# Kernel optimization log

Measured on AMD Instinct MI355X. Metric: run time of the kernel, lower is better.

The kernel has to match this reference:

```python
import jax, jax.numpy as jnp
import numpy as np
import math

B, T, C = 2, 2048, 2048
H = 16
HS = C // H            # 128
NLQ = 512              # q latent dim
NLKV = 512             # kv latent dim
RHD = 64               # rope head dim


def _rope(x, cos, sin):
    # x: [B,T,H,D], cos/sin: [T,D/2]; rotate consecutive pairs (re,im)
    b, t, h, d = x.shape
    xr = x.reshape(b, t, h, d // 2, 2)
    x_re, x_im = xr[..., 0], xr[..., 1]
    c = cos[None, :, None, :]
    s = sin[None, :, None, :]
    o_re = x_re * c - x_im * s
    o_im = x_re * s + x_im * c
    return jnp.stack([o_re, o_im], axis=-1).reshape(b, t, h, d)


def setup_inputs() -> dict:
    key = jax.random.key(0)
    ks = jax.random.split(key, 9)
    std = 0.02
    x = jax.random.normal(ks[0], (B, T, C), dtype=jnp.float32)
    # RoPE tables (rotary base 10000) for rope_head_dim
    inv_freq = 1.0 / (10000.0 ** (np.arange(0, RHD, 2, dtype=np.float32) / RHD))
    tpos = np.arange(T, dtype=np.float32)
    ang = np.outer(tpos, inv_freq)  # [T, RHD/2]
    freqs_cos = jnp.asarray(np.cos(ang), dtype=jnp.float32)
    freqs_sin = jnp.asarray(np.sin(ang), dtype=jnp.float32)
    W_dq = std * jax.random.normal(ks[1], (NLQ, C), dtype=jnp.float32)
    W_uq = std * jax.random.normal(ks[2], (C, NLQ), dtype=jnp.float32)
    W_dkv = std * jax.random.normal(ks[3], (NLKV, C), dtype=jnp.float32)
    W_uk = std * jax.random.normal(ks[4], (C, NLKV), dtype=jnp.float32)
    W_uv = std * jax.random.normal(ks[5], (C, NLKV), dtype=jnp.float32)
    W_qr = std * jax.random.normal(ks[6], (H * RHD, NLQ), dtype=jnp.float32)
    W_kr = std * jax.random.normal(ks[7], (RHD, C), dtype=jnp.float32)
    W_o = std * jax.random.normal(ks[8], (C, C), dtype=jnp.float32)
    return {"x": x, "freqs_cos": freqs_cos, "freqs_sin": freqs_sin,
            "W_dq": W_dq, "W_uq": W_uq, "W_dkv": W_dkv, "W_uk": W_uk,
            "W_uv": W_uv, "W_qr": W_qr, "W_kr": W_kr, "W_o": W_o}


def reference(x, freqs_cos, freqs_sin, W_dq, W_uq, W_dkv, W_uk, W_uv, W_qr, W_kr, W_o):
    b, t, c = x.shape
    # latent projections
    c_q = x @ W_dq.T                                   # [B,T,NLQ]
    q_c = (c_q @ W_uq.T).reshape(b, t, H, HS)          # content query
    c_kv = x @ W_dkv.T                                 # [B,T,NLKV]
    k_c = (c_kv @ W_uk.T).reshape(b, t, H, HS)         # content key
    v = (c_kv @ W_uv.T).reshape(b, t, H, HS)           # value
    # decoupled RoPE parts
    q_r = _rope((c_q @ W_qr.T).reshape(b, t, H, RHD), freqs_cos, freqs_sin)
    k_r = _rope((x @ W_kr.T).reshape(b, t, 1, RHD), freqs_cos, freqs_sin)
    k_r = jnp.broadcast_to(k_r, (b, t, H, RHD))        # shared across heads
    q = jnp.concatenate([q_c, q_r], axis=-1)           # [B,T,H,HS+RHD]
    k = jnp.concatenate([k_c, k_r], axis=-1)
    scale = 1.0 / math.sqrt(HS + RHD)
    scores = jnp.einsum('bqhd,bkhd->bhqk', q, k) * scale
    mask = jnp.tril(jnp.ones((t, t), dtype=bool))
    scores = jnp.where(mask[None, None], scores, jnp.finfo(scores.dtype).min)
    attn = jax.nn.softmax(scores, axis=-1)
    out = jnp.einsum('bhqk,bkhd->bqhd', attn, v).reshape(b, t, c)
    return out @ W_o.T
```

## Files before the change

### kernel.cpp

```cpp
#include <hip/hip_runtime.h>
#include <math.h>

#define B_ 2
#define T_ 2048
#define C_ 2048
#define H_ 16
#define HS_ 128
#define RHD_ 64

typedef _Float16 f16;
typedef f16 half8 __attribute__((ext_vector_type(8)));
typedef f16 half4v __attribute__((ext_vector_type(4)));
typedef f16 half2v __attribute__((ext_vector_type(2)));
typedef float f32x4 __attribute__((ext_vector_type(4)));

using gvoid_t = const __attribute__((address_space(1))) void;
using lvoid_t = __attribute__((address_space(3))) void;

#define GLOAD_LDS(gp, lp) \
  __builtin_amdgcn_global_load_lds((gvoid_t*)(gp), (lvoid_t*)(lp), 16, 0, 0)

struct ConvBatch {
  const float* src[9];
  f16* dst[9];
  int n[9];
};

__global__ __launch_bounds__(256) void conv_f32_f16_batch(ConvBatch args) {
  const int t = blockIdx.y;
  const float* __restrict__ s = args.src[t];
  f16* __restrict__ d = args.dst[t];
  const int n4 = args.n[t] >> 2;
  for (int i = blockIdx.x * blockDim.x + threadIdx.x; i < n4;
       i += gridDim.x * blockDim.x) {
    float4 v = ((const float4*)s)[i];
    half4v h = {(f16)v.x, (f16)v.y, (f16)v.z, (f16)v.w};
    ((half4v*)d)[i] = h;
  }
}

template <int BM, int BN, bool OUTF32>
__global__ __launch_bounds__(256) void gemm_nt(const f16* __restrict__ A,
                                               const f16* __restrict__ Bw,
                                               void* __restrict__ Cv, int M,
                                               int N, int K, float alpha) {
  constexpr int MF = BM / 32;
  constexpr int NF = BN / 32;
  __shared__ f16 As[2][BM * 32];
  __shared__ f16 Bs[2][BN * 32];
  const int tid = threadIdx.x;
  const int wid = tid >> 6;
  const int lane = tid & 63;
  const int l15 = lane & 15, lg = lane >> 4;
  const int wr = wid >> 1, wc = wid & 1;
  const long bm = (long)blockIdx.y * BM;
  const long bn = (long)blockIdx.x * BN;

  const f16* Ag = A + (bm + (tid >> 2)) * (long)K + (tid & 3) * 8;
  const f16* Bg = Bw + (bn + (tid >> 2)) * (long)K + (tid & 3) * 8;

  auto stg = [&](int p, int k0) {
#pragma unroll
    for (int c = 0; c < BM / 64; ++c)
      GLOAD_LDS(Ag + (long)c * 64 * K + k0, &As[p][wid * 512 + c * 2048]);
#pragma unroll
    for (int c = 0; c < BN / 64; ++c)
      GLOAD_LDS(Bg + (long)c * 64 * K + k0, &Bs[p][wid * 512 + c * 2048]);
  };

  f32x4 acc[MF][NF];
  const f32x4 zero = {0.f, 0.f, 0.f, 0.f};
#pragma unroll
  for (int m = 0; m < MF; ++m)
#pragma unroll
    for (int n = 0; n < NF; ++n) acc[m][n] = zero;

  stg(0, 0);
  __syncthreads();

  int cur = 0;
  for (int k0 = 0; k0 < K; k0 += 32) {
    if (k0 + 32 < K) stg(cur ^ 1, k0 + 32);
    half8 af[MF], bf[NF];
#pragma unroll
    for (int m = 0; m < MF; ++m)
      af[m] =
          *(const half8*)&As[cur][(wr * (BM / 2) + m * 16 + l15) * 32 + lg * 8];
#pragma unroll
    for (int n = 0; n < NF; ++n)
      bf[n] =
          *(const half8*)&Bs[cur][(wc * (BN / 2) + n * 16 + l15) * 32 + lg * 8];
    __builtin_amdgcn_s_setprio(1);
#pragma unroll
    for (int m = 0; m < MF; ++m)
#pragma unroll
      for (int n = 0; n < NF; ++n)
        acc[m][n] =
            __builtin_amdgcn_mfma_f32_16x16x32_f16(af[m], bf[n], acc[m][n], 0, 0, 0);
    __builtin_amdgcn_s_setprio(0);
    __syncthreads();
    cur ^= 1;
  }

#pragma unroll
  for (int m = 0; m < MF; ++m) {
#pragma unroll
    for (int n = 0; n < NF; ++n) {
#pragma unroll
      for (int r = 0; r < 4; ++r) {
        long row = bm + wr * (BM / 2) + m * 16 + lg * 4 + r;
        long col = bn + wc * (BN / 2) + n * 16 + l15;
        float v = acc[m][n][r] * alpha;
        if constexpr (OUTF32)
          ((float*)Cv)[row * N + col] = v;
        else
          ((f16*)Cv)[row * N + col] = (f16)v;
      }
    }
  }
}

__global__ __launch_bounds__(256) void rope_q_kernel(
    const f16* __restrict__ src, const float* __restrict__ cs,
    const float* __restrict__ sn, f16* __restrict__ dst, float scale) {
  int idx = blockIdx.x * blockDim.x + threadIdx.x;
  if (idx >= B_ * T_ * H_ * 32) return;
  int j = idx & 31;
  int t = (idx >> 9) & (T_ - 1);
  half2v v = *(const half2v*)(src + (size_t)idx * 2);
  float c = cs[t * 32 + j], s = sn[t * 32 + j];
  float re = (float)v[0], im = (float)v[1];
  half2v o2 = {(f16)((re * c - im * s) * scale),
               (f16)((re * s + im * c) * scale)};
  *(half2v*)(dst + (size_t)idx * 2) = o2;
}

__global__ __launch_bounds__(256) void rope_k_kernel(
    const f16* __restrict__ src, const float* __restrict__ cs,
    const float* __restrict__ sn, f16* __restrict__ dst) {
  int idx = blockIdx.x * blockDim.x + threadIdx.x;
  if (idx >= B_ * T_ * 32) return;
  int j = idx & 31;
  int t = (idx >> 5) & (T_ - 1);
  half2v v = *(const half2v*)(src + (size_t)idx * 2);
  float c = cs[t * 32 + j], s = sn[t * 32 + j];
  float re = (float)v[0], im = (float)v[1];
  half2v o2 = {(f16)(re * c - im * s), (f16)(re * s + im * c)};
  *(half2v*)(dst + (size_t)idx * 2) = o2;
}

__global__ __launch_bounds__(256) void transpose_v_kernel(
    const f16* __restrict__ v, f16* __restrict__ vt) {
  __shared__ f16 tile[64][64];
  const int t0 = blockIdx.x * 64, d0 = blockIdx.y * 64;
  const int bh = blockIdx.z, b = bh >> 4, h = bh & 15;
  const int rr = threadIdx.x >> 3, cc = (threadIdx.x & 7) * 8;
#pragma unroll
  for (int p = 0; p < 2; ++p) {
    int r = rr + p * 32;
    int sc = (((cc >> 3) ^ ((r >> 3) & 7)) << 3);
    *(half8*)&tile[r][sc] =
        *(const half8*)&v[(((size_t)(b * T_ + t0 + r) * H_ + h) * HS_) + d0 + cc];
  }
  __syncthreads();
#pragma unroll
  for (int p = 0; p < 2; ++p) {
    int d = rr + p * 32;
    half8 o;
#pragma unroll
    for (int jj = 0; jj < 8; ++jj) {
      int row = cc + jj;
      o[jj] = tile[row][((((d >> 3) ^ ((row >> 3) & 7)) << 3) | (d & 7))];
    }
    *(half8*)&vt[((size_t)bh * HS_ + d0 + d) * T_ + t0 + cc] = o;
  }
}

__global__ __launch_bounds__(256) void attn_fwd(
    const f16* __restrict__ qc, const f16* __restrict__ qr,
    const f16* __restrict__ kc, const f16* __restrict__ kr,
    const f16* __restrict__ vt, f16* __restrict__ outp) {
  __shared__ f16 KcS[2][4096];
  __shared__ f16 KrS[2][2048];
  __shared__ f16 VsS[2][4096];
  __shared__ f16 Ps[4][576];

  const int tid = threadIdx.x;
  const int wid = tid >> 6, lane = tid & 63;
  const int l15 = lane & 15, lg = lane >> 4;
  const int lid = blockIdx.x;
  const int pj = lid & 15;
  const int bh = lid >> 4;
  const int b = bh >> 4, h = bh & 15;
  const size_t bT = (size_t)b * T_;
  const f16* Vb = vt + (size_t)bh * HS_ * T_;
  const f32x4 zero = {0.f, 0.f, 0.f, 0.f};

  const f16* sbase[5];
  long sinc[5];
  char* d0[5];
  char* d1[5];
#pragma unroll
  for (int i = 0; i < 5; ++i) {
    const int g = wid * 5 + i;
    if (g < 8) {
      int ofs = g * 1024 + lane * 16;
      int row = ofs >> 8, c = ofs & 255;
      int cs = c ^ ((row & 7) << 4);
      sbase[i] = kc + (bT + row) * (long)C_ + h * HS_ + (cs >> 1);
      sinc[i] = 32 * (long)C_;
      d0[i] = (char*)KcS[0] + g * 1024;
      d1[i] = (char*)KcS[1] + g * 1024;
    } else if (g < 12) {
      int g2 = g - 8;
      int ofs = g2 * 1024 + lane * 16;
      int row = ofs >> 7, c = ofs & 127;
      int cs = c ^ ((row & 7) << 4);
      sbase[i] = kr + (bT + row) * (long)RHD_ + (cs >> 1);
      sinc[i] = 32 * (long)RHD_;
      d0[i] = (char*)KrS[0] + g2 * 1024;
      d1[i] = (char*)KrS[1] + g2 * 1024;
    } else {
      int g3 = g - 12;
      int ofs = g3 * 1024 + lane * 16;
      int row = ofs >> 6, c = ofs & 63;
      int cs = c ^ ((row & 3) << 4);
      sbase[i] = Vb + (long)row * T_ + (cs >> 1);
      sinc[i] = 32;
      d0[i] = (char*)VsS[0] + g3 * 1024;
      d1[i] = (char*)VsS[1] + g3 * 1024;
    }
  }

  char* Pw = (char*)Ps[wid];

  for (int sidx = 0; sidx < 2; ++sidx) {
    const int qtile = sidx ? (31 - pj) : pj;
    const int qs = qtile * 64 + wid * 16;
    const int nt = 2 * qtile + 2;

    const f16* sp[5];
#pragma unroll
    for (int i = 0; i < 5; ++i) sp[i] = sbase[i];
#pragma unroll
    for (int i = 0; i < 5; ++i) {
      GLOAD_LDS(sp[i], d0[i]);
      sp[i] += sinc[i];
    }

    half8 qf[6];
    {
      const size_t bq = bT + qs + l15;
      const f16* pc = qc + bq * C_ + h * HS_ + lg * 8;
#pragma unroll
      for (int ks = 0; ks < 4; ++ks) qf[ks] = *(const half8*)(pc + ks * 32);
      const f16* pr = qr + bq * (H_ * RHD_) + h * RHD_ + lg * 8;
#pragma unroll
      for (int ks = 0; ks < 2; ++ks) qf[4 + ks] = *(const half8*)(pr + ks * 32);
    }

    f32x4 o[8];
#pragma unroll
    for (int n = 0; n < 8; ++n) o[n] = zero;
    float m_r = -3e38f, l_r = 0.f;

    __syncthreads();

    for (int it = 0; it < nt; ++it) {
      const int kt = it * 32;
      const int cur = it & 1;
      if (it + 1 < nt) {
#pragma unroll
        for (int i = 0; i < 5; ++i) {
          GLOAD_LDS(sp[i], cur ? d0[i] : d1[i]);
          sp[i] += sinc[i];
        }
      }

      if (kt <= qs + 15) {
        const char* kcb = (const char*)KcS[cur];
        const char* krb = (const char*)KrS[cur];
        const char* vsb = (const char*)VsS[cur];

        f32x4 s[2] = {zero, zero};
        __builtin_amdgcn_s_setprio(1);
#pragma unroll
        for (int a2 = 0; a2 < 2; ++a2) {
          const int row = a2 * 16 + l15;
          const int sw = (row & 7) << 4;
          const char* pk = kcb + (row << 8);
#pragma unroll
          for (int ks = 0; ks < 4; ++ks) {
            half8 kf = *(const half8*)(pk + ((ks * 64 + lg * 16) ^ sw));
            s[a2] = __builtin_amdgcn_mfma_f32_16x16x32_f16(kf, qf[ks], s[a2], 0, 0, 0);
          }
          const char* pk2 = krb + (row << 7);
#pragma unroll
          for (int ks = 0; ks < 2; ++ks) {
            half8 kf = *(const half8*)(pk2 + ((ks * 64 + lg * 16) ^ sw));
            s[a2] = __builtin_amdgcn_mfma_f32_16x16x32_f16(kf, qf[4 + ks], s[a2], 0,
                                                           0, 0);
          }
        }
        __builtin_amdgcn_s_setprio(0);

        if (kt + 31 > qs) {
#pragma unroll
          for (int a2 = 0; a2 < 2; ++a2)
#pragma unroll
            for (int r = 0; r < 4; ++r) {
              int key = kt + a2 * 16 + lg * 4 + r;
              if (key > qs + l15) s[a2][r] = -1e30f;
            }
        }

        float mx = fmaxf(fmaxf(fmaxf(s[0][0], s[0][1]), fmaxf(s[0][2], s[0][3])),
                         fmaxf(fmaxf(s[1][0], s[1][1]), fmaxf(s[1][2], s[1][3])));
        mx = fmaxf(mx, __shfl_xor(mx, 16));
        mx = fmaxf(mx, __shfl_xor(mx, 32));
        if (!__all(mx <= m_r + 8.f)) {
          float mn = fmaxf(m_r, mx);
          float corr = __expf(m_r - mn);
          m_r = mn;
          l_r *= corr;
#pragma unroll
          for (int r = 0; r < 4; ++r) {
            float cb =
                __shfl(corr, (lane & 48) | (((lane >> 4) & 3) << 2) | r);
#pragma unroll
            for (int n = 0; n < 8; ++n) o[n][r] *= cb;
          }
        }
        float ps = 0.f;
#pragma unroll
        for (int a2 = 0; a2 < 2; ++a2) {
          half4v p4;
#pragma unroll
          for (int r = 0; r < 4; ++r) {
            float p = __expf(s[a2][r] - m_r);
            ps += p;
            p4[r] = (f16)p;
          }
          *(half4v*)(Pw + l15 * 72 + a2 * 32 + lg * 8) = p4;
        }
        l_r += ps;

        half8 pa = *(const half8*)(Pw + l15 * 72 + lg * 16);
        __builtin_amdgcn_s_setprio(1);
#pragma unroll
        for (int n = 0; n < 8; ++n) {
          const int row = n * 16 + l15;
          half8 vb = *(const half8*)(vsb + (row << 6) +
                                     ((lg * 16) ^ ((row & 3) << 4)));
          o[n] = __builtin_amdgcn_mfma_f32_16x16x32_f16(pa, vb, o[n], 0, 0, 0);
        }
        __builtin_amdgcn_s_setprio(0);
      }
      __syncthreads();
    }

    float lt = l_r;
    lt += __shfl_xor(lt, 16);
    lt += __shfl_xor(lt, 32);
#pragma unroll
    for (int r = 0; r < 4; ++r) {
      float lb = __shfl(lt, (lane & 48) | (((lane >> 4) & 3) << 2) | r);
      float inv = 1.f / lb;
      size_t rowb = (bT + qs + lg * 4 + r) * (size_t)C_ + h * HS_ + l15;
#pragma unroll
      for (int n = 0; n < 8; ++n) outp[rowb + n * 16] = (f16)(o[n][r] * inv);
    }
  }
}

extern "C" void kernel_launch(void* const* d_in, const int* in_sizes, int n_in,
                              void* d_out, int out_size, void* d_ws,
                              size_t ws_size, hipStream_t stream) {
  const float* x = (const float*)d_in[0];
  const float* fcos = (const float*)d_in[1];
  const float* fsin = (const float*)d_in[2];
  const float* W_dq = (const float*)d_in[3];
  const float* W_uq = (const float*)d_in[4];
  const float* W_dkv = (const float*)d_in[5];
  const float* W_uk = (const float*)d_in[6];
  const float* W_uv = (const float*)d_in[7];
  const float* W_qr = (const float*)d_in[8];
  const float* W_kr = (const float*)d_in[9];
  const float* W_o = (const float*)d_in[10];

  char* ws = (char*)d_ws;
  size_t off = 0;
  auto alc = [&](size_t elems) {
    f16* p = (f16*)(ws + off);
    off += ((elems * 2 + 255) & ~(size_t)255);
    return p;
  };
  const size_t MT = (size_t)B_ * T_;
  f16* xb = alc(MT * 2048);
  f16* wdq = alc((size_t)512 * 2048);
  f16* wuq = alc((size_t)2048 * 512);
  f16* wdkv = alc((size_t)512 * 2048);
  f16* wuk = alc((size_t)2048 * 512);
  f16* wuv = alc((size_t)2048 * 512);
  f16* wqr = alc((size_t)1024 * 512);
  f16* wkr = alc((size_t)64 * 2048);
  f16* wo = alc((size_t)2048 * 2048);
  f16* c_q = alc(MT * 512);
  f16* c_kv = alc(MT * 512);
  f16* q_cb = alc(MT * 2048);
  f16* qr_raw = alc(MT * 1024);
  f16* q_rb = alc(MT * 1024);
  f16* k_cb = alc(MT * 2048);
  f16* kr_raw = alc(MT * 64);
  f16* k_rb = alc(MT * 64);
  f16* vb = alc(MT * 2048);
  f16* vtb = alc(MT * 2048);
  f16* aout = alc(MT * 2048);

  ConvBatch cb;
  cb.src[0] = x;     cb.dst[0] = xb;   cb.n[0] = (int)(MT * 2048);
  cb.src[1] = W_dq;  cb.dst[1] = wdq;  cb.n[1] = 512 * 2048;
  cb.src[2] = W_uq;  cb.dst[2] = wuq;  cb.n[2] = 2048 * 512;
  cb.src[3] = W_dkv; cb.dst[3] = wdkv; cb.n[3] = 512 * 2048;
  cb.src[4] = W_uk;  cb.dst[4] = wuk;  cb.n[4] = 2048 * 512;
  cb.src[5] = W_uv;  cb.dst[5] = wuv;  cb.n[5] = 2048 * 512;
  cb.src[6] = W_qr;  cb.dst[6] = wqr;  cb.n[6] = 1024 * 512;
  cb.src[7] = W_kr;  cb.dst[7] = wkr;  cb.n[7] = 64 * 2048;
  cb.src[8] = W_o;   cb.dst[8] = wo;   cb.n[8] = 2048 * 2048;
  conv_f32_f16_batch<<<dim3(128, 9), 256, 0, stream>>>(cb);

  const float scale = 0.07216878364870323f;

  gemm_nt<128, 64, false><<<dim3(8, 32), 256, 0, stream>>>(
      xb, wdq, c_q, 4096, 512, 2048, 1.f);
  gemm_nt<128, 64, false><<<dim3(8, 32), 256, 0, stream>>>(
      xb, wdkv, c_kv, 4096, 512, 2048, 1.f);
  gemm_nt<64, 64, false><<<dim3(1, 64), 256, 0, stream>>>(
      xb, wkr, kr_raw, 4096, 64, 2048, 1.f);
  gemm_nt<128, 128, false><<<dim3(16, 32), 256, 0, stream>>>(
      c_q, wuq, q_cb, 4096, 2048, 512, scale);
  gemm_nt<128, 128, false><<<dim3(8, 32), 256, 0, stream>>>(
      c_q, wqr, qr_raw, 4096, 1024, 512, 1.f);
  gemm_nt<128, 128, false><<<dim3(16, 32), 256, 0, stream>>>(
      c_kv, wuk, k_cb, 4096, 2048, 512, 1.f);
  gemm_nt<128, 128, false><<<dim3(16, 32), 256, 0, stream>>>(
      c_kv, wuv, vb, 4096, 2048, 512, 1.f);

  rope_q_kernel<<<(B_ * T_ * H_ * 32) / 256, 256, 0, stream>>>(
      qr_raw, fcos, fsin, q_rb, scale);
  rope_k_kernel<<<(B_ * T_ * 32) / 256, 256, 0, stream>>>(kr_raw, fcos, fsin,
                                                          k_rb);
  transpose_v_kernel<<<dim3(T_ / 64, 2, B_ * H_), 256, 0, stream>>>(vb, vtb);

  attn_fwd<<<dim3(512), 256, 0, stream>>>(q_cb, q_rb, k_cb, k_rb, vtb, aout);

  gemm_nt<128, 128, true><<<dim3(16, 32), 256, 0, stream>>>(
      aout, wo, d_out, 4096, 2048, 2048, 1.f);
}
```

Before: 465.6 us.

## Concatenate projection weights to merge seven GEMMs into three with swizzled tiles

Packs W_dq, W_dkv and W_kr into one down-projection weight, W_uq/W_qr into one q up-projection and W_uk/W_uv into one kv up-projection. This cuts the projection GEMM launches from seven to three and reads x once instead of three times. Downstream kernels now read from strided column slices. The attention scale moves into the fp16 weight conversion, and a block-index swizzle is added to group tiles for L2 reuse. The down GEMM now computes 1152 columns, so the kr part is padded out to a full 128-wide tile.

```diff
diff --git a/kernel.cpp b/kernel.cpp
--- a/kernel.cpp
+++ b/kernel.cpp
@@ -8,6 +8,10 @@
 #define HS_ 128
 #define RHD_ 64
 
+#define LD_DOWN 1152
+#define LD_UPQ 3072
+#define LD_UPKV 4096
+
 typedef _Float16 f16;
 typedef f16 half8 __attribute__((ext_vector_type(8)));
 typedef f16 half4v __attribute__((ext_vector_type(4)));
@@ -24,26 +28,30 @@
   const float* src[9];
   f16* dst[9];
   int n[9];
+  float scl[9];
 };
 
 __global__ __launch_bounds__(256) void conv_f32_f16_batch(ConvBatch args) {
   const int t = blockIdx.y;
   const float* __restrict__ s = args.src[t];
   f16* __restrict__ d = args.dst[t];
+  const float sc = args.scl[t];
   const int n4 = args.n[t] >> 2;
   for (int i = blockIdx.x * blockDim.x + threadIdx.x; i < n4;
        i += gridDim.x * blockDim.x) {
     float4 v = ((const float4*)s)[i];
-    half4v h = {(f16)v.x, (f16)v.y, (f16)v.z, (f16)v.w};
+    half4v h = {(f16)(v.x * sc), (f16)(v.y * sc), (f16)(v.z * sc),
+                (f16)(v.w * sc)};
     ((half4v*)d)[i] = h;
   }
 }
 
 template <int BM, int BN, bool OUTF32>
 __global__ __launch_bounds__(256) void gemm_nt(const f16* __restrict__ A,
+                                               long lda,
                                                const f16* __restrict__ Bw,
-                                               void* __restrict__ Cv, int M,
-                                               int N, int K, float alpha) {
+                                               void* __restrict__ Cv, long ldc,
+                                               int K, int gx) {
   constexpr int MF = BM / 32;
   constexpr int NF = BN / 32;
   __shared__ f16 As[2][BM * 32];
@@ -53,16 +61,20 @@
   const int lane = tid & 63;
   const int l15 = lane & 15, lg = lane >> 4;
   const int wr = wid >> 1, wc = wid & 1;
-  const long bm = (long)blockIdx.y * BM;
-  const long bn = (long)blockIdx.x * BN;
-
-  const f16* Ag = A + (bm + (tid >> 2)) * (long)K + (tid & 3) * 8;
+
+  const int nwg = gridDim.x;
+  const int cpx = nwg >> 3;
+  const int swz = (blockIdx.x & 7) * cpx + (blockIdx.x >> 3);
+  const long bm = (long)(swz / gx) * BM;
+  const long bn = (long)(swz % gx) * BN;
+
+  const f16* Ag = A + (bm + (tid >> 2)) * lda + (tid & 3) * 8;
   const f16* Bg = Bw + (bn + (tid >> 2)) * (long)K + (tid & 3) * 8;
 
   auto stg = [&](int p, int k0) {
 #pragma unroll
     for (int c = 0; c < BM / 64; ++c)
-      GLOAD_LDS(Ag + (long)c * 64 * K + k0, &As[p][wid * 512 + c * 2048]);
+      GLOAD_LDS(Ag + (long)c * 64 * lda + k0, &As[p][wid * 512 + c * 2048]);
 #pragma unroll
     for (int c = 0; c < BN / 64; ++c)
       GLOAD_LDS(Bg + (long)c * 64 * K + k0, &Bs[p][wid * 512 + c * 2048]);
@@ -110,11 +122,11 @@
       for (int r = 0; r < 4; ++r) {
         long row = bm + wr * (BM / 2) + m * 16 + lg * 4 + r;
         long col = bn + wc * (BN / 2) + n * 16 + l15;
-        float v = acc[m][n][r] * alpha;
+        float v = acc[m][n][r];
         if constexpr (OUTF32)
-          ((float*)Cv)[row * N + col] = v;
+          ((float*)Cv)[row * ldc + col] = v;
         else
-          ((f16*)Cv)[row * N + col] = (f16)v;
+          ((f16*)Cv)[row * ldc + col] = (f16)v;
       }
     }
   }
@@ -126,8 +138,10 @@
   int idx = blockIdx.x * blockDim.x + threadIdx.x;
   if (idx >= B_ * T_ * H_ * 32) return;
   int j = idx & 31;
-  int t = (idx >> 9) & (T_ - 1);
-  half2v v = *(const half2v*)(src + (size_t)idx * 2);
+  int ta = idx >> 9;
+  int t = ta & (T_ - 1);
+  int rem = idx & 511;
+  half2v v = *(const half2v*)(src + (size_t)ta * LD_UPQ + 2048 + rem * 2);
   float c = cs[t * 32 + j], s = sn[t * 32 + j];
   float re = (float)v[0], im = (float)v[1];
   half2v o2 = {(f16)((re * c - im * s) * scale),
@@ -141,8 +155,9 @@
   int idx = blockIdx.x * blockDim.x + threadIdx.x;
   if (idx >= B_ * T_ * 32) return;
   int j = idx & 31;
-  int t = (idx >> 5) & (T_ - 1);
-  half2v v = *(const half2v*)(src + (size_t)idx * 2);
+  int ta = idx >> 5;
+  int t = ta & (T_ - 1);
+  half2v v = *(const half2v*)(src + (size_t)ta * LD_DOWN + 1024 + j * 2);
   float c = cs[t * 32 + j], s = sn[t * 32 + j];
   float re = (float)v[0], im = (float)v[1];
   half2v o2 = {(f16)(re * c - im * s), (f16)(re * s + im * c)};
@@ -159,8 +174,9 @@
   for (int p = 0; p < 2; ++p) {
     int r = rr + p * 32;
     int sc = (((cc >> 3) ^ ((r >> 3) & 7)) << 3);
-    *(half8*)&tile[r][sc] =
-        *(const half8*)&v[(((size_t)(b * T_ + t0 + r) * H_ + h) * HS_) + d0 + cc];
+    *(half8*)&tile[r][sc] = *(const half8*)&v[(size_t)(b * T_ + t0 + r) *
+                                                  LD_UPKV +
+                                              2048 + h * HS_ + d0 + cc];
   }
   __syncthreads();
 #pragma unroll
@@ -207,8 +223,8 @@
       int ofs = g * 1024 + lane * 16;
       int row = ofs >> 8, c = ofs & 255;
       int cs = c ^ ((row & 7) << 4);
-      sbase[i] = kc + (bT + row) * (long)C_ + h * HS_ + (cs >> 1);
-      sinc[i] = 32 * (long)C_;
+      sbase[i] = kc + (bT + row) * (long)LD_UPKV + h * HS_ + (cs >> 1);
+      sinc[i] = 32 * (long)LD_UPKV;
       d0[i] = (char*)KcS[0] + g * 1024;
       d1[i] = (char*)KcS[1] + g * 1024;
     } else if (g < 12) {
@@ -251,7 +267,7 @@
     half8 qf[6];
     {
       const size_t bq = bT + qs + l15;
-      const f16* pc = qc + bq * C_ + h * HS_ + lg * 8;
+      const f16* pc = qc + bq * LD_UPQ + h * HS_ + lg * 8;
 #pragma unroll
       for (int ks = 0; ks < 4; ++ks) qf[ks] = *(const half8*)(pc + ks * 32);
       const f16* pr = qr + bq * (H_ * RHD_) + h * RHD_ + lg * 8;
@@ -397,63 +413,48 @@
   };
   const size_t MT = (size_t)B_ * T_;
   f16* xb = alc(MT * 2048);
-  f16* wdq = alc((size_t)512 * 2048);
-  f16* wuq = alc((size_t)2048 * 512);
-  f16* wdkv = alc((size_t)512 * 2048);
-  f16* wuk = alc((size_t)2048 * 512);
-  f16* wuv = alc((size_t)2048 * 512);
-  f16* wqr = alc((size_t)1024 * 512);
-  f16* wkr = alc((size_t)64 * 2048);
+  f16* wdown = alc((size_t)LD_DOWN * 2048);
+  f16* wupq = alc((size_t)LD_UPQ * 512);
+  f16* wupkv = alc((size_t)LD_UPKV * 512);
   f16* wo = alc((size_t)2048 * 2048);
-  f16* c_q = alc(MT * 512);
-  f16* c_kv = alc(MT * 512);
-  f16* q_cb = alc(MT * 2048);
-  f16* qr_raw = alc(MT * 1024);
+  f16* cdown = alc(MT * LD_DOWN);
+  f16* upq = alc(MT * LD_UPQ);
+  f16* upkv = alc(MT * LD_UPKV);
   f16* q_rb = alc(MT * 1024);
-  f16* k_cb = alc(MT * 2048);
-  f16* kr_raw = alc(MT * 64);
   f16* k_rb = alc(MT * 64);
-  f16* vb = alc(MT * 2048);
   f16* vtb = alc(MT * 2048);
   f16* aout = alc(MT * 2048);
 
+  const float scale = 0.07216878364870323f;
+
   ConvBatch cb;
-  cb.src[0] = x;     cb.dst[0] = xb;   cb.n[0] = (int)(MT * 2048);
-  cb.src[1] = W_dq;  cb.dst[1] = wdq;  cb.n[1] = 512 * 2048;
-  cb.src[2] = W_uq;  cb.dst[2] = wuq;  cb.n[2] = 2048 * 512;
-  cb.src[3] = W_dkv; cb.dst[3] = wdkv; cb.n[3] = 512 * 2048;
-  cb.src[4] = W_uk;  cb.dst[4] = wuk;  cb.n[4] = 2048 * 512;
-  cb.src[5] = W_uv;  cb.dst[5] = wuv;  cb.n[5] = 2048 * 512;
-  cb.src[6] = W_qr;  cb.dst[6] = wqr;  cb.n[6] = 1024 * 512;
-  cb.src[7] = W_kr;  cb.dst[7] = wkr;  cb.n[7] = 64 * 2048;
-  cb.src[8] = W_o;   cb.dst[8] = wo;   cb.n[8] = 2048 * 2048;
+  cb.src[0] = x;     cb.dst[0] = xb;                  cb.n[0] = (int)(MT * 2048); cb.scl[0] = 1.f;
+  cb.src[1] = W_dq;  cb.dst[1] = wdown;               cb.n[1] = 512 * 2048;       cb.scl[1] = 1.f;
+  cb.src[2] = W_dkv; cb.dst[2] = wdown + 512 * 2048;  cb.n[2] = 512 * 2048;       cb.scl[2] = 1.f;
+  cb.src[3] = W_kr;  cb.dst[3] = wdown + 1024 * 2048; cb.n[3] = 64 * 2048;        cb.scl[3] = 1.f;
+  cb.src[4] = W_uq;  cb.dst[4] = wupq;                cb.n[4] = 2048 * 512;       cb.scl[4] = scale;
+  cb.src[5] = W_qr;  cb.dst[5] = wupq + 2048 * 512;   cb.n[5] = 1024 * 512;       cb.scl[5] = 1.f;
+  cb.src[6] = W_uk;  cb.dst[6] = wupkv;               cb.n[6] = 2048 * 512;       cb.scl[6] = 1.f;
+  cb.src[7] = W_uv;  cb.dst[7] = wupkv + 2048 * 512;  cb.n[7] = 2048 * 512;       cb.scl[7] = 1.f;
+  cb.src[8] = W_o;   cb.dst[8] = wo;                  cb.n[8] = 2048 * 2048;      cb.scl[8] = 1.f;
   conv_f32_f16_batch<<<dim3(128, 9), 256, 0, stream>>>(cb);
 
-  const float scale = 0.07216878364870323f;
-
-  gemm_nt<128, 64, false><<<dim3(8, 32), 256, 0, stream>>>(
-      xb, wdq, c_q, 4096, 512, 2048, 1.f);
-  gemm_nt<128, 64, false><<<dim3(8, 32), 256, 0, stream>>>(
-      xb, wdkv, c_kv, 4096, 512, 2048, 1.f);
-  gemm_nt<64, 64, false><<<dim3(1, 64), 256, 0, stream>>>(
-      xb, wkr, kr_raw, 4096, 64, 2048, 1.f);
-  gemm_nt<128, 128, false><<<dim3(16, 32), 256, 0, stream>>>(
-      c_q, wuq, q_cb, 4096, 2048, 512, scale);
-  gemm_nt<128, 128, false><<<dim3(8, 32), 256, 0, stream>>>(
-      c_q, wqr, qr_raw, 4096, 1024, 512, 1.f);
-  gemm_nt<128, 128, false><<<dim3(16, 32), 256, 0, stream>>>(
-      c_kv, wuk, k_cb, 4096, 2048, 512, 1.f);
-  gemm_nt<128, 128, false><<<dim3(16, 32), 256, 0, stream>>>(
-      c_kv, wuv, vb, 4096, 2048, 512, 1.f);
+  gemm_nt<128, 128, false><<<288, 256, 0, stream>>>(xb, 2048, wdown, cdown,
+                                                    LD_DOWN, 2048, 9);
+  gemm_nt<128, 128, false><<<768, 256, 0, stream>>>(cdown, LD_DOWN, wupq, upq,
+                                                    LD_UPQ, 512, 24);
+  gemm_nt<128, 128, false><<<1024, 256, 0, stream>>>(cdown + 512, LD_DOWN,
+                                                     wupkv, upkv, LD_UPKV, 512,
+                                                     32);
 
   rope_q_kernel<<<(B_ * T_ * H_ * 32) / 256, 256, 0, stream>>>(
-      qr_raw, fcos, fsin, q_rb, scale);
-  rope_k_kernel<<<(B_ * T_ * 32) / 256, 256, 0, stream>>>(kr_raw, fcos, fsin,
+      upq, fcos, fsin, q_rb, scale);
+  rope_k_kernel<<<(B_ * T_ * 32) / 256, 256, 0, stream>>>(cdown, fcos, fsin,
                                                           k_rb);
-  transpose_v_kernel<<<dim3(T_ / 64, 2, B_ * H_), 256, 0, stream>>>(vb, vtb);
-
-  attn_fwd<<<dim3(512), 256, 0, stream>>>(q_cb, q_rb, k_cb, k_rb, vtb, aout);
-
-  gemm_nt<128, 128, true><<<dim3(16, 32), 256, 0, stream>>>(
-      aout, wo, d_out, 4096, 2048, 2048, 1.f);
-}
+  transpose_v_kernel<<<dim3(T_ / 64, 2, B_ * H_), 256, 0, stream>>>(upkv, vtb);
+
+  attn_fwd<<<dim3(512), 256, 0, stream>>>(upq, q_rb, upkv, k_rb, vtb, aout);
+
+  gemm_nt<128, 128, true><<<512, 256, 0, stream>>>(aout, 2048, wo, d_out, 2048,
+                                                   2048, 16);
+}
```

After: 415.8 us. 10.7% less time.
